# Kernel tuning notes

Measured on AMD Instinct MI355X. Metric: run time of the kernel, lower is better.

## Reference

```python
import jax, jax.numpy as jnp
import numpy as np

DT = 0.1          # sampling interval
DJ = 0.125        # scale resolution
W0 = 6.0          # Morlet omega0 (f0=6 -> deltaj0=0.6 in module)
DELTAJ0 = 0.6
WINDOW = 32
WS = WINDOW * 3 - 2  # sliding window size = 94

# rect window used in scale-smoothing (pycwt.rect): ones with half-weight ends, normalized
_wsize = int(round(DELTAJ0 / DJ * 2))  # 10
_win = np.ones(_wsize, np.float32)
_win[0] = _win[-1] = 0.5
_win /= _win.sum()


def _scales(n):
    # Morlet minimum scale s.t. Fourier period == 2*dt (wavelets_pytorch convention)
    s0 = 2.0 * DT * (W0 + np.sqrt(2.0 + W0 ** 2)) / (4.0 * np.pi)
    J = int((1.0 / DJ) * np.log2(n * DT / s0))
    return (s0 * 2.0 ** (DJ * np.arange(J + 1))).astype(np.float32)


def _cwt(y, scales, nfft):
    # Torrence & Compo FFT-based Morlet CWT. y: [n] real -> [S, n] complex
    n = y.shape[0]
    w = (2.0 * np.pi * np.fft.fftfreq(nfft, d=DT)).astype(np.float32)
    yh = jnp.fft.fft(y, n=nfft)                                  # [nfft]
    sw = scales[:, None] * w[None, :]                            # [S, nfft]
    psi_hat = (np.pi ** -0.25) * jnp.exp(-0.5 * (sw - W0) ** 2) * (w[None, :] > 0)
    norm = jnp.sqrt(2.0 * np.pi * scales[:, None] / DT)          # unit-energy normalization
    return jnp.fft.ifft(yh[None, :] * (norm * psi_hat), axis=1)[:, :n]


def _smooth(Wm, scales, nfft, real):
    # time smoothing: Gaussian filter in Fourier domain per scale (padded fft)
    n = Wm.shape[1]
    k2 = ((2.0 * np.pi * np.fft.fftfreq(nfft)).astype(np.float32)) ** 2
    F = jnp.exp(-0.5 * (scales[:, None] / DT) ** 2 * k2[None, :])  # [S, nfft]
    T = jnp.fft.ifft(F * jnp.fft.fft(Wm, n=nfft, axis=1), axis=1)[:, :n]
    if real:
        T = T.real
    # scale smoothing: boxcar-with-half-ends, 'same' convolution along scale axis
    win = jnp.asarray(_win).astype(T.dtype)
    return jax.vmap(lambda col: jnp.convolve(col, win, mode='same'),
                    in_axes=1, out_axes=1)(T)


def _wct(y1, y2, scales, nfft):
    y1 = (y1 - y1.mean()) / y1.std()
    y2 = (y2 - y2.mean()) / y2.std()
    W1 = _cwt(y1, scales, nfft)
    W2 = _cwt(y2, scales, nfft)
    inv_s = 1.0 / scales[:, None]
    S1 = _smooth(jnp.abs(W1) ** 2 * inv_s, scales, nfft, real=True)
    S2 = _smooth(jnp.abs(W2) ** 2 * inv_s, scales, nfft, real=True)
    S12 = _smooth(W1 * jnp.conj(W2) * inv_s, scales, nfft, real=False)
    wct = jnp.abs(S12) ** 2 / (S1 * S2)
    return wct.sum(axis=0)  # [n] coherence summed over scales


def setup_inputs() -> dict:
    key = jax.random.key(0)
    x = jax.random.normal(key, (64, 2, 2048), dtype=jnp.float32)
    return {"x": x}


def reference(x):
    n = x.shape[-1]
    nfft = int(2 ** np.ceil(np.log2(n)))  # pycwt fft_kwargs: next power of two
    scales = jnp.asarray(_scales(n))
    coh = jax.vmap(lambda p: _wct(p[0], p[1], scales, nfft))(x)   # [B, n]
    # sliding-window sum (unfold(0, WS, 1).sum(dim=1)) via cumsum
    cs = jnp.pad(jnp.cumsum(coh, axis=1), ((0, 0), (1, 0)))
    return cs[:, WS:] - cs[:, :-WS]                               # [B, n - WS + 1]
```

## Files before the change

kernel.cpp:

```cpp
#include <hip/hip_runtime.h>
#include <math.h>

#define N        2048
#define NT       256
#define NSC      81
#define BATCH    64
#define WS_WIN   94
#define NOUT     1955
#define DT_S     0.1f
#define W0_C     6.0f
#define PI_F     3.14159265358979f
#define TWOPI_F  6.28318530717959f
#define PIM14    0.7511255444649425f
#define C_SQ2H   0.70710678118654752f

#define SWZ(e)   ((e) + ((e) >> 4))
#define LDSN     2176

typedef float f4v __attribute__((ext_vector_type(4)));

__device__ __forceinline__ float4 ntload4(const float4* p) {
    f4v t = __builtin_nontemporal_load((const f4v*)p);
    return make_float4(t.x, t.y, t.z, t.w);
}
__device__ __forceinline__ void ntstore4(float4* p, float4 v) {
    f4v t; t.x = v.x; t.y = v.y; t.z = v.z; t.w = v.w;
    __builtin_nontemporal_store(t, (f4v*)p);
}

__device__ __forceinline__ float2 cadd2(float2 a, float2 b) { return make_float2(a.x + b.x, a.y + b.y); }
__device__ __forceinline__ float2 csub2(float2 a, float2 b) { return make_float2(a.x - b.x, a.y - b.y); }
__device__ __forceinline__ float2 cmul2(float2 a, float2 b) { return make_float2(a.x * b.x - a.y * b.y, a.x * b.y + a.y * b.x); }

struct Tw { float2 w[3][7]; };

__device__ __forceinline__ void tw_init(Tw& tw, int tid) {
    const int jm0 = tid, jm1 = tid & ~7, jm2 = tid & ~63;
    const int jms[3] = { jm0, jm1, jm2 };
    #pragma unroll
    for (int t = 0; t < 3; ++t) {
        float ang = -(TWOPI_F / (float)N) * (float)jms[t];
        float sn, cs; __sincosf(ang, &sn, &cs);
        float2 w1 = make_float2(cs, sn);
        tw.w[t][0] = w1;
        #pragma unroll
        for (int p = 1; p < 7; ++p) tw.w[t][p] = cmul2(tw.w[t][p - 1], w1);
    }
}

template<int SGN>
__device__ __forceinline__ float2 cmul_tw(float2 a, float2 w) {
    if (SGN < 0) return make_float2(a.x * w.x - a.y * w.y, a.x * w.y + a.y * w.x);
    else         return make_float2(a.x * w.x + a.y * w.y, a.y * w.x - a.x * w.y);
}

template<int SGN, bool HALF>
__device__ __forceinline__ void dft8(const float2 (&x)[8], float2 (&y)[8]) {
    const float s = (float)SGN;
    float2 t0, t1, t2, t3, u0, d1, d2, d3;
    if (HALF) {
        t0 = x[0]; t1 = x[1]; t2 = x[2]; t3 = x[3];
        u0 = x[0]; d1 = x[1]; d2 = x[2]; d3 = x[3];
    } else {
        t0 = cadd2(x[0], x[4]); t1 = cadd2(x[1], x[5]);
        t2 = cadd2(x[2], x[6]); t3 = cadd2(x[3], x[7]);
        u0 = csub2(x[0], x[4]);
        d1 = csub2(x[1], x[5]);
        d2 = csub2(x[2], x[6]);
        d3 = csub2(x[3], x[7]);
    }
    float2 u1 = make_float2(C_SQ2H * (d1.x - s * d1.y), C_SQ2H * (d1.y + s * d1.x));
    float2 u2 = make_float2(-s * d2.y, s * d2.x);
    float2 u3 = make_float2(-C_SQ2H * (d3.x + s * d3.y), C_SQ2H * (s * d3.x - d3.y));
    float2 a0 = cadd2(t0, t2), a1 = cadd2(t1, t3), b0 = csub2(t0, t2), e1 = csub2(t1, t3);
    float2 b1 = make_float2(-s * e1.y, s * e1.x);
    y[0] = cadd2(a0, a1); y[4] = csub2(a0, a1); y[2] = cadd2(b0, b1); y[6] = csub2(b0, b1);
    float2 c0 = cadd2(u0, u2), c1 = cadd2(u1, u3), g0 = csub2(u0, u2), h1 = csub2(u1, u3);
    float2 g1 = make_float2(-s * h1.y, s * h1.x);
    y[1] = cadd2(c0, c1); y[5] = csub2(c0, c1); y[3] = cadd2(g0, g1); y[7] = csub2(g0, g1);
}

template<int SGN>
__device__ __forceinline__ void twiddle_store(const float2 (&y)[8], float2* __restrict__ dst,
                                              const float2 (&w)[7], int base, int m) {
    dst[SWZ(base)] = y[0];
    #pragma unroll
    for (int p = 1; p < 8; ++p)
        dst[SWZ(base + p * m)] = cmul_tw<SGN>(y[p], w[p - 1]);
}

template<int SGN, bool HALF>
__device__ __forceinline__ void stage1_reg(const float2 (&x)[8], float2* __restrict__ dst,
                                           const Tw& tw, int tid) {
    float2 y[8];
    dft8<SGN, HALF>(x, y);
    twiddle_store<SGN>(y, dst, tw.w[0], 8 * tid, 1);
}

__device__ __forceinline__ void stage_read(const float2* __restrict__ src, float2 (&x)[8], int q) {
    #pragma unroll
    for (int p = 0; p < 8; ++p) x[p] = src[SWZ(q + p * 256)];
}

template<int SGN, int TWS>
__device__ __forceinline__ void stage_write(float2* __restrict__ dst, const float2 (&x)[8],
                                            const Tw& tw, int q) {
    float2 y[8];
    dft8<SGN, false>(x, y);
    const int m  = (TWS == 1) ? 8 : 64;
    const int jm = q & ~(m - 1);
    twiddle_store<SGN>(y, dst, tw.w[TWS], q + 7 * jm, m);
}

template<int SGN>
__device__ __forceinline__ void stage4_regs(const float2* __restrict__ src, float2 (&x)[8], int tid) {
    const float s = (float)SGN;
    #pragma unroll
    for (int qq = 0; qq < 2; ++qq) {
        int q = tid + qq * 256;
        float2 x0 = src[SWZ(q)];
        float2 x1 = src[SWZ(q + 512)];
        float2 x2 = src[SWZ(q + 1024)];
        float2 x3 = src[SWZ(q + 1536)];
        float2 a0 = cadd2(x0, x2), a1 = cadd2(x1, x3);
        float2 b0 = csub2(x0, x2), e1 = csub2(x1, x3);
        float2 b1 = make_float2(-s * e1.y, s * e1.x);
        x[0 + qq] = cadd2(a0, a1);
        x[2 + qq] = cadd2(b0, b1);
        x[4 + qq] = csub2(a0, a1);
        x[6 + qq] = csub2(b0, b1);
    }
}

template<int SGN, bool HALF>
__device__ __forceinline__ void fft2048_dual(float2 (&u)[8], float2 (&v)[8],
                                             float2* U, float2* V, const Tw& tw, int tid) {
    __syncthreads();
    stage1_reg<SGN, HALF>(u, U, tw, tid);
    stage1_reg<SGN, HALF>(v, V, tw, tid);
    __syncthreads();
    float2 xu[8], xv[8];
    stage_read(U, xu, tid);
    stage_read(V, xv, tid);
    __syncthreads();
    stage_write<SGN, 1>(U, xu, tw, tid);
    stage_write<SGN, 1>(V, xv, tw, tid);
    __syncthreads();
    stage_read(U, xu, tid);
    stage_read(V, xv, tid);
    __syncthreads();
    stage_write<SGN, 2>(U, xu, tw, tid);
    stage_write<SGN, 2>(V, xv, tw, tid);
    __syncthreads();
    stage4_regs<SGN>(U, u, tid);
    stage4_regs<SGN>(V, v, tid);
}

template<int SGN>
__device__ __forceinline__ void fft2048_single(float2 (&u)[8], float2* U, const Tw& tw, int tid) {
    __syncthreads();
    stage1_reg<SGN, false>(u, U, tw, tid);
    __syncthreads();
    float2 x[8];
    stage_read(U, x, tid);
    __syncthreads();
    stage_write<SGN, 1>(U, x, tw, tid);
    __syncthreads();
    stage_read(U, x, tid);
    __syncthreads();
    stage_write<SGN, 2>(U, x, tw, tid);
    __syncthreads();
    stage4_regs<SGN>(U, u, tid);
}

__global__ __launch_bounds__(NT) void k_fft_in(const float* __restrict__ x,
                                               float2* __restrict__ spec) {
    __shared__ float2 A[LDSN];
    __shared__ float  rs[NT], rq[NT];
    const int    tid = threadIdx.x;
    const float* y   = x + (size_t)blockIdx.x * N;

    Tw tw; tw_init(tw, tid);

    float v[8];
    float lsum = 0.f, lsq = 0.f;
    #pragma unroll
    for (int i = 0; i < 8; ++i) {
        float t = y[tid + i * NT];
        v[i] = t; lsum += t; lsq += t * t;
    }
    rs[tid] = lsum; rq[tid] = lsq;
    __syncthreads();
    for (int o = NT / 2; o > 0; o >>= 1) {
        if (tid < o) { rs[tid] += rs[tid + o]; rq[tid] += rq[tid + o]; }
        __syncthreads();
    }
    const float mean = rs[0] * (1.f / N);
    const float var  = rq[0] * (1.f / N) - mean * mean;
    const float inv  = rsqrtf(var);

    float2 z[8];
    #pragma unroll
    for (int i = 0; i < 8; ++i) z[i] = make_float2((v[i] - mean) * inv, 0.f);

    fft2048_single<-1>(z, A, tw, tid);

    float2* o2 = spec + (size_t)blockIdx.x * N;
    #pragma unroll
    for (int i = 0; i < 8; ++i) o2[tid + i * NT] = z[i];
}

__global__ __launch_bounds__(NT, 3) void k_wct(const float2* __restrict__ spec,
                                               float4* __restrict__ T, int b0) {
    __shared__ float2 U[LDSN];
    __shared__ float2 V[LDSN];
    const int tid  = threadIdx.x;
    const int sidx = blockIdx.x % NSC;
    const int bl   = blockIdx.x / NSC;
    const int b    = b0 + bl;

    Tw tw; tw_init(tw, tid);

    const float s0    = 2.f * DT_S * (W0_C + sqrtf(2.f + W0_C * W0_C)) / (4.f * PI_F);
    const float s     = s0 * exp2f(0.125f * (float)sidx);
    const float inv_s = 1.f / s;

    const float2* yh1 = spec + (size_t)(b * 2 + 0) * N;
    const float2* yh2 = spec + (size_t)(b * 2 + 1) * N;

    const float nrm   = PIM14 * sqrtf(TWOPI_F * s / DT_S) * (1.f / N);
    const float wstep = TWOPI_F / ((float)N * DT_S);

    float2 w1[8], w2[8];
    #pragma unroll
    for (int i = 0; i < 4; ++i) {
        int   k = tid + i * NT;
        float f = 0.f;
        if (k >= 1) {
            float arg = s * (wstep * (float)k) - W0_C;
            f = nrm * expf(-0.5f * arg * arg);
        }
        float2 a = yh1[k];
        float2 c = yh2[k];
        w1[i] = make_float2(a.x * f, a.y * f);
        w2[i] = make_float2(c.x * f, c.y * f);
    }
    #pragma unroll
    for (int i = 4; i < 8; ++i) {
        w1[i] = make_float2(0.f, 0.f);
        w2[i] = make_float2(0.f, 0.f);
    }
    fft2048_dual<+1, true>(w1, w2, U, V, tw, tid);

    float2 P[8], C[8];
    #pragma unroll
    for (int i = 0; i < 8; ++i) {
        float2 a = w1[i], c = w2[i];
        P[i] = make_float2((a.x * a.x + a.y * a.y) * inv_s,
                           (c.x * c.x + c.y * c.y) * inv_s);
        C[i] = make_float2((a.x * c.x + a.y * c.y) * inv_s,
                           (a.y * c.x - a.x * c.y) * inv_s);
    }

    const float sdt = s / DT_S;
    const float fc  = -0.5f * sdt * sdt * (TWOPI_F / (float)N) * (TWOPI_F / (float)N);

    fft2048_dual<-1, false>(P, C, U, V, tw, tid);

    #pragma unroll
    for (int i = 0; i < 8; ++i) {
        int   k  = tid + i * NT;
        int   mk = min(k, N - k);
        float F  = expf(fc * (float)(mk * mk)) * (1.f / N);
        P[i].x *= F; P[i].y *= F;
        C[i].x *= F; C[i].y *= F;
    }

    fft2048_dual<+1, false>(P, C, U, V, tw, tid);

    float4* To = T + ((size_t)bl * NSC + sidx) * N;
    #pragma unroll
    for (int i = 0; i < 8; ++i) {
        int k = tid + i * NT;
        ntstore4(&To[k], make_float4(P[i].x, P[i].y, C[i].x, C[i].y));
    }
}

__global__ __launch_bounds__(NT) void k_coh(const float4* __restrict__ T,
                                            float* __restrict__ coh, int b0) {
    const int bl = blockIdx.x >> 3;
    const int t  = ((blockIdx.x & 7) << 8) + threadIdx.x;
    const int b  = b0 + bl;
    const float4* col = T + (size_t)bl * NSC * N + t;

    float4 q[10];
    #pragma unroll
    for (int i = 0; i < 10; ++i) q[i] = make_float4(0.f, 0.f, 0.f, 0.f);
    #pragma unroll
    for (int i = 0; i < 5; ++i) q[5 + i] = ntload4(&col[(size_t)i * N]);

    float acc = 0.f;
    const float w9 = 1.f / 9.f;
    for (int i = 0; i < NSC; ++i) {
        float sx = 0.f, sy = 0.f, sz = 0.f, sw = 0.f;
        #pragma unroll
        for (int k = 0; k < 10; ++k) { sx += q[k].x; sy += q[k].y; sz += q[k].z; sw += q[k].w; }
        float s1 = (sx - 0.5f * (q[0].x + q[9].x)) * w9;
        float s2 = (sy - 0.5f * (q[0].y + q[9].y)) * w9;
        float sr = (sz - 0.5f * (q[0].z + q[9].z)) * w9;
        float si = (sw - 0.5f * (q[0].w + q[9].w)) * w9;
        acc += (sr * sr + si * si) / (s1 * s2);
        #pragma unroll
        for (int k = 0; k < 9; ++k) q[k] = q[k + 1];
        int c = i + 5;
        q[9] = (c < NSC) ? ntload4(&col[(size_t)c * N]) : make_float4(0.f, 0.f, 0.f, 0.f);
    }
    coh[(size_t)b * N + t] = acc;
}

__global__ __launch_bounds__(NT) void k_win(const float* __restrict__ coh,
                                            float* __restrict__ out) {
    __shared__ float row[N];
    const int b   = blockIdx.x;
    const int tid = threadIdx.x;
    for (int i = tid; i < N; i += NT) row[i] = coh[(size_t)b * N + i];
    __syncthreads();
    for (int t0 = tid; t0 < NOUT; t0 += NT) {
        float ssum = 0.f;
        for (int k = 0; k < WS_WIN; ++k) ssum += row[t0 + k];
        out[(size_t)b * NOUT + t0] = ssum;
    }
}

extern "C" void kernel_launch(void* const* d_in, const int* in_sizes, int n_in,
                              void* d_out, int out_size, void* d_ws, size_t ws_size,
                              hipStream_t stream) {
    const float* x   = (const float*)d_in[0];
    float*       out = (float*)d_out;
    char*        ws  = (char*)d_ws;

    const size_t spec_bytes = (size_t)BATCH * 2 * N * sizeof(float2);
    const size_t coh_bytes  = (size_t)BATCH * N * sizeof(float);
    const size_t perBatchT  = (size_t)NSC * N * sizeof(float4);

    float2* spec = (float2*)ws;
    float*  coh  = (float*)(ws + spec_bytes);
    float4* T    = (float4*)(ws + spec_bytes + coh_bytes);

    size_t avail = (ws_size > spec_bytes + coh_bytes) ? (ws_size - spec_bytes - coh_bytes) : 0;
    int chunk = (int)(avail / perBatchT);
    if (chunk < 1) chunk = 1;
    if (chunk > BATCH) chunk = BATCH;

    k_fft_in<<<BATCH * 2, NT, 0, stream>>>(x, spec);
    for (int b0 = 0; b0 < BATCH; b0 += chunk) {
        int cb = BATCH - b0 < chunk ? BATCH - b0 : chunk;
        k_wct<<<cb * NSC, NT, 0, stream>>>(spec, T, b0);
        k_coh<<<cb * 8, NT, 0, stream>>>(T, coh, b0);
    }
    k_win<<<BATCH, NT, 0, stream>>>(coh, out);
}
```

Baseline: 187.8 us.

## Vectorize complex math, split coherence scale loop, use prefix-sum sliding window

Complex arithmetic is rewritten with 2-wide float vectors so the compiler can emit packed FP32 ops in the FFTs. The k_coh scale loop is split into two halves per column, doubling the block count, with a deeper prefetch queue; the two partial sums go to separate buffers. k_win now builds a block-wide prefix sum and takes differences instead of summing 94 elements per output, and the input-normalization reduction uses wave shuffles. Together these target low occupancy in k_coh and redundant work in the small kernels, at the cost of extra workspace and a second coherence buffer.

```diff
diff --git a/kernel.cpp b/kernel.cpp
--- a/kernel.cpp
+++ b/kernel.cpp
@@ -18,6 +18,7 @@
 #define LDSN     2176
 
 typedef float f4v __attribute__((ext_vector_type(4)));
+typedef float f2 __attribute__((ext_vector_type(2)));
 
 __device__ __forceinline__ float4 ntload4(const float4* p) {
     f4v t = __builtin_nontemporal_load((const f4v*)p);
@@ -28,61 +29,68 @@
     __builtin_nontemporal_store(t, (f4v*)p);
 }
 
-__device__ __forceinline__ float2 cadd2(float2 a, float2 b) { return make_float2(a.x + b.x, a.y + b.y); }
-__device__ __forceinline__ float2 csub2(float2 a, float2 b) { return make_float2(a.x - b.x, a.y - b.y); }
-__device__ __forceinline__ float2 cmul2(float2 a, float2 b) { return make_float2(a.x * b.x - a.y * b.y, a.x * b.y + a.y * b.x); }
-
-struct Tw { float2 w[3][7]; };
+__device__ __forceinline__ f2 shxx(f2 a) { return __builtin_shufflevector(a, a, 0, 0); }
+__device__ __forceinline__ f2 shyy(f2 a) { return __builtin_shufflevector(a, a, 1, 1); }
+__device__ __forceinline__ f2 shyx(f2 a) { return __builtin_shufflevector(a, a, 1, 0); }
+
+template<int SGN>
+__device__ __forceinline__ f2 rot90(f2 d) {
+    return shyx(d) * (f2){ -(float)SGN, (float)SGN };
+}
+
+__device__ __forceinline__ f2 cmul(f2 a, f2 b) {
+    f2 t = shxx(a) * b;
+    f2 u = shyy(a) * shyx(b);
+    return t + u * (f2){ -1.f, 1.f };
+}
+
+template<int SGN>
+__device__ __forceinline__ f2 cmul_tw(f2 a, f2 w) {
+    f2 t = shxx(a) * w;
+    f2 u = shyy(a) * shyx(w);
+    if (SGN < 0) return t + u * (f2){ -1.f, 1.f };
+    else         return u + t * (f2){ 1.f, -1.f };
+}
+
+struct Tw { f2 w[3][7]; };
 
 __device__ __forceinline__ void tw_init(Tw& tw, int tid) {
-    const int jm0 = tid, jm1 = tid & ~7, jm2 = tid & ~63;
-    const int jms[3] = { jm0, jm1, jm2 };
+    const int jms[3] = { tid, tid & ~7, tid & ~63 };
     #pragma unroll
     for (int t = 0; t < 3; ++t) {
         float ang = -(TWOPI_F / (float)N) * (float)jms[t];
         float sn, cs; __sincosf(ang, &sn, &cs);
-        float2 w1 = make_float2(cs, sn);
+        f2 w1 = { cs, sn };
         tw.w[t][0] = w1;
         #pragma unroll
-        for (int p = 1; p < 7; ++p) tw.w[t][p] = cmul2(tw.w[t][p - 1], w1);
-    }
-}
-
-template<int SGN>
-__device__ __forceinline__ float2 cmul_tw(float2 a, float2 w) {
-    if (SGN < 0) return make_float2(a.x * w.x - a.y * w.y, a.x * w.y + a.y * w.x);
-    else         return make_float2(a.x * w.x + a.y * w.y, a.y * w.x - a.x * w.y);
+        for (int p = 1; p < 7; ++p) tw.w[t][p] = cmul(tw.w[t][p - 1], w1);
+    }
 }
 
 template<int SGN, bool HALF>
-__device__ __forceinline__ void dft8(const float2 (&x)[8], float2 (&y)[8]) {
-    const float s = (float)SGN;
-    float2 t0, t1, t2, t3, u0, d1, d2, d3;
+__device__ __forceinline__ void dft8(const f2 (&x)[8], f2 (&y)[8]) {
+    f2 t0, t1, t2, t3, u0, d1, d2, d3;
     if (HALF) {
         t0 = x[0]; t1 = x[1]; t2 = x[2]; t3 = x[3];
         u0 = x[0]; d1 = x[1]; d2 = x[2]; d3 = x[3];
     } else {
-        t0 = cadd2(x[0], x[4]); t1 = cadd2(x[1], x[5]);
-        t2 = cadd2(x[2], x[6]); t3 = cadd2(x[3], x[7]);
-        u0 = csub2(x[0], x[4]);
-        d1 = csub2(x[1], x[5]);
-        d2 = csub2(x[2], x[6]);
-        d3 = csub2(x[3], x[7]);
-    }
-    float2 u1 = make_float2(C_SQ2H * (d1.x - s * d1.y), C_SQ2H * (d1.y + s * d1.x));
-    float2 u2 = make_float2(-s * d2.y, s * d2.x);
-    float2 u3 = make_float2(-C_SQ2H * (d3.x + s * d3.y), C_SQ2H * (s * d3.x - d3.y));
-    float2 a0 = cadd2(t0, t2), a1 = cadd2(t1, t3), b0 = csub2(t0, t2), e1 = csub2(t1, t3);
-    float2 b1 = make_float2(-s * e1.y, s * e1.x);
-    y[0] = cadd2(a0, a1); y[4] = csub2(a0, a1); y[2] = cadd2(b0, b1); y[6] = csub2(b0, b1);
-    float2 c0 = cadd2(u0, u2), c1 = cadd2(u1, u3), g0 = csub2(u0, u2), h1 = csub2(u1, u3);
-    float2 g1 = make_float2(-s * h1.y, s * h1.x);
-    y[1] = cadd2(c0, c1); y[5] = csub2(c0, c1); y[3] = cadd2(g0, g1); y[7] = csub2(g0, g1);
+        t0 = x[0] + x[4]; t1 = x[1] + x[5]; t2 = x[2] + x[6]; t3 = x[3] + x[7];
+        u0 = x[0] - x[4]; d1 = x[1] - x[5]; d2 = x[2] - x[6]; d3 = x[3] - x[7];
+    }
+    f2 u1 = (d1 + rot90<SGN>(d1)) * C_SQ2H;
+    f2 u2 = rot90<SGN>(d2);
+    f2 u3 = (rot90<SGN>(d3) - d3) * C_SQ2H;
+    f2 a0 = t0 + t2, a1 = t1 + t3, b0 = t0 - t2, e1 = t1 - t3;
+    f2 b1 = rot90<SGN>(e1);
+    y[0] = a0 + a1; y[4] = a0 - a1; y[2] = b0 + b1; y[6] = b0 - b1;
+    f2 c0 = u0 + u2, c1 = u1 + u3, g0 = u0 - u2, h1 = u1 - u3;
+    f2 g1 = rot90<SGN>(h1);
+    y[1] = c0 + c1; y[5] = c0 - c1; y[3] = g0 + g1; y[7] = g0 - g1;
 }
 
 template<int SGN>
-__device__ __forceinline__ void twiddle_store(const float2 (&y)[8], float2* __restrict__ dst,
-                                              const float2 (&w)[7], int base, int m) {
+__device__ __forceinline__ void twiddle_store(const f2 (&y)[8], f2* __restrict__ dst,
+                                              const f2 (&w)[7], int base, int m) {
     dst[SWZ(base)] = y[0];
     #pragma unroll
     for (int p = 1; p < 8; ++p)
@@ -90,22 +98,22 @@
 }
 
 template<int SGN, bool HALF>
-__device__ __forceinline__ void stage1_reg(const float2 (&x)[8], float2* __restrict__ dst,
+__device__ __forceinline__ void stage1_reg(const f2 (&x)[8], f2* __restrict__ dst,
                                            const Tw& tw, int tid) {
-    float2 y[8];
+    f2 y[8];
     dft8<SGN, HALF>(x, y);
     twiddle_store<SGN>(y, dst, tw.w[0], 8 * tid, 1);
 }
 
-__device__ __forceinline__ void stage_read(const float2* __restrict__ src, float2 (&x)[8], int q) {
+__device__ __forceinline__ void stage_read(const f2* __restrict__ src, f2 (&x)[8], int q) {
     #pragma unroll
     for (int p = 0; p < 8; ++p) x[p] = src[SWZ(q + p * 256)];
 }
 
 template<int SGN, int TWS>
-__device__ __forceinline__ void stage_write(float2* __restrict__ dst, const float2 (&x)[8],
+__device__ __forceinline__ void stage_write(f2* __restrict__ dst, const f2 (&x)[8],
                                             const Tw& tw, int q) {
-    float2 y[8];
+    f2 y[8];
     dft8<SGN, false>(x, y);
     const int m  = (TWS == 1) ? 8 : 64;
     const int jm = q & ~(m - 1);
@@ -113,33 +121,31 @@
 }
 
 template<int SGN>
-__device__ __forceinline__ void stage4_regs(const float2* __restrict__ src, float2 (&x)[8], int tid) {
-    const float s = (float)SGN;
+__device__ __forceinline__ void stage4_regs(const f2* __restrict__ src, f2 (&x)[8], int tid) {
     #pragma unroll
     for (int qq = 0; qq < 2; ++qq) {
         int q = tid + qq * 256;
-        float2 x0 = src[SWZ(q)];
-        float2 x1 = src[SWZ(q + 512)];
-        float2 x2 = src[SWZ(q + 1024)];
-        float2 x3 = src[SWZ(q + 1536)];
-        float2 a0 = cadd2(x0, x2), a1 = cadd2(x1, x3);
-        float2 b0 = csub2(x0, x2), e1 = csub2(x1, x3);
-        float2 b1 = make_float2(-s * e1.y, s * e1.x);
-        x[0 + qq] = cadd2(a0, a1);
-        x[2 + qq] = cadd2(b0, b1);
-        x[4 + qq] = csub2(a0, a1);
-        x[6 + qq] = csub2(b0, b1);
+        f2 x0 = src[SWZ(q)];
+        f2 x1 = src[SWZ(q + 512)];
+        f2 x2 = src[SWZ(q + 1024)];
+        f2 x3 = src[SWZ(q + 1536)];
+        f2 a0 = x0 + x2, a1 = x1 + x3, b0 = x0 - x2, e1 = x1 - x3;
+        f2 b1 = rot90<SGN>(e1);
+        x[0 + qq] = a0 + a1;
+        x[2 + qq] = b0 + b1;
+        x[4 + qq] = a0 - a1;
+        x[6 + qq] = b0 - b1;
     }
 }
 
 template<int SGN, bool HALF>
-__device__ __forceinline__ void fft2048_dual(float2 (&u)[8], float2 (&v)[8],
-                                             float2* U, float2* V, const Tw& tw, int tid) {
+__device__ __forceinline__ void fft2048_dual(f2 (&u)[8], f2 (&v)[8],
+                                             f2* U, f2* V, const Tw& tw, int tid) {
     __syncthreads();
     stage1_reg<SGN, HALF>(u, U, tw, tid);
     stage1_reg<SGN, HALF>(v, V, tw, tid);
     __syncthreads();
-    float2 xu[8], xv[8];
+    f2 xu[8], xv[8];
     stage_read(U, xu, tid);
     stage_read(V, xv, tid);
     __syncthreads();
@@ -157,11 +163,11 @@
 }
 
 template<int SGN>
-__device__ __forceinline__ void fft2048_single(float2 (&u)[8], float2* U, const Tw& tw, int tid) {
+__device__ __forceinline__ void fft2048_single(f2 (&u)[8], f2* U, const Tw& tw, int tid) {
     __syncthreads();
     stage1_reg<SGN, false>(u, U, tw, tid);
     __syncthreads();
-    float2 x[8];
+    f2 x[8];
     stage_read(U, x, tid);
     __syncthreads();
     stage_write<SGN, 1>(U, x, tw, tid);
@@ -174,9 +180,9 @@
 }
 
 __global__ __launch_bounds__(NT) void k_fft_in(const float* __restrict__ x,
-                                               float2* __restrict__ spec) {
-    __shared__ float2 A[LDSN];
-    __shared__ float  rs[NT], rq[NT];
+                                               f2* __restrict__ spec) {
+    __shared__ f2 A[LDSN];
+    __shared__ float rs[4], rq[4];
     const int    tid = threadIdx.x;
     const float* y   = x + (size_t)blockIdx.x * N;
 
@@ -189,31 +195,35 @@
         float t = y[tid + i * NT];
         v[i] = t; lsum += t; lsq += t * t;
     }
-    rs[tid] = lsum; rq[tid] = lsq;
-    __syncthreads();
-    for (int o = NT / 2; o > 0; o >>= 1) {
-        if (tid < o) { rs[tid] += rs[tid + o]; rq[tid] += rq[tid + o]; }
-        __syncthreads();
-    }
-    const float mean = rs[0] * (1.f / N);
-    const float var  = rq[0] * (1.f / N) - mean * mean;
+    #pragma unroll
+    for (int o = 1; o < 64; o <<= 1) {
+        lsum += __shfl_xor(lsum, o, 64);
+        lsq  += __shfl_xor(lsq,  o, 64);
+    }
+    const int wid = tid >> 6, lane = tid & 63;
+    if (lane == 0) { rs[wid] = lsum; rq[wid] = lsq; }
+    __syncthreads();
+    const float fsum = rs[0] + rs[1] + rs[2] + rs[3];
+    const float fsq  = rq[0] + rq[1] + rq[2] + rq[3];
+    const float mean = fsum * (1.f / N);
+    const float var  = fsq * (1.f / N) - mean * mean;
     const float inv  = rsqrtf(var);
 
-    float2 z[8];
-    #pragma unroll
-    for (int i = 0; i < 8; ++i) z[i] = make_float2((v[i] - mean) * inv, 0.f);
+    f2 z[8];
+    #pragma unroll
+    for (int i = 0; i < 8; ++i) z[i] = (f2){ (v[i] - mean) * inv, 0.f };
 
     fft2048_single<-1>(z, A, tw, tid);
 
-    float2* o2 = spec + (size_t)blockIdx.x * N;
+    f2* o2 = spec + (size_t)blockIdx.x * N;
     #pragma unroll
     for (int i = 0; i < 8; ++i) o2[tid + i * NT] = z[i];
 }
 
-__global__ __launch_bounds__(NT, 3) void k_wct(const float2* __restrict__ spec,
+__global__ __launch_bounds__(NT, 3) void k_wct(const f2* __restrict__ spec,
                                                float4* __restrict__ T, int b0) {
-    __shared__ float2 U[LDSN];
-    __shared__ float2 V[LDSN];
+    __shared__ f2 U[LDSN];
+    __shared__ f2 V[LDSN];
     const int tid  = threadIdx.x;
     const int sidx = blockIdx.x % NSC;
     const int bl   = blockIdx.x / NSC;
@@ -225,13 +235,13 @@
     const float s     = s0 * exp2f(0.125f * (float)sidx);
     const float inv_s = 1.f / s;
 
-    const float2* yh1 = spec + (size_t)(b * 2 + 0) * N;
-    const float2* yh2 = spec + (size_t)(b * 2 + 1) * N;
+    const f2* yh1 = spec + (size_t)(b * 2 + 0) * N;
+    const f2* yh2 = spec + (size_t)(b * 2 + 1) * N;
 
     const float nrm   = PIM14 * sqrtf(TWOPI_F * s / DT_S) * (1.f / N);
     const float wstep = TWOPI_F / ((float)N * DT_S);
 
-    float2 w1[8], w2[8];
+    f2 w1[8], w2[8];
     #pragma unroll
     for (int i = 0; i < 4; ++i) {
         int   k = tid + i * NT;
@@ -240,26 +250,23 @@
             float arg = s * (wstep * (float)k) - W0_C;
             f = nrm * expf(-0.5f * arg * arg);
         }
-        float2 a = yh1[k];
-        float2 c = yh2[k];
-        w1[i] = make_float2(a.x * f, a.y * f);
-        w2[i] = make_float2(c.x * f, c.y * f);
+        w1[i] = yh1[k] * f;
+        w2[i] = yh2[k] * f;
     }
     #pragma unroll
     for (int i = 4; i < 8; ++i) {
-        w1[i] = make_float2(0.f, 0.f);
-        w2[i] = make_float2(0.f, 0.f);
+        w1[i] = (f2){ 0.f, 0.f };
+        w2[i] = (f2){ 0.f, 0.f };
     }
     fft2048_dual<+1, true>(w1, w2, U, V, tw, tid);
 
-    float2 P[8], C[8];
+    f2 P[8], C[8];
     #pragma unroll
     for (int i = 0; i < 8; ++i) {
-        float2 a = w1[i], c = w2[i];
-        P[i] = make_float2((a.x * a.x + a.y * a.y) * inv_s,
-                           (c.x * c.x + c.y * c.y) * inv_s);
-        C[i] = make_float2((a.x * c.x + a.y * c.y) * inv_s,
-                           (a.y * c.x - a.x * c.y) * inv_s);
+        f2 a = w1[i], c = w2[i];
+        f2 aa = a * a, cc = c * c;
+        P[i] = (f2){ aa.x + aa.y, cc.x + cc.y } * inv_s;
+        C[i] = cmul_tw<+1>(a, c) * inv_s;
     }
 
     const float sdt = s / DT_S;
@@ -272,8 +279,8 @@
         int   k  = tid + i * NT;
         int   mk = min(k, N - k);
         float F  = expf(fc * (float)(mk * mk)) * (1.f / N);
-        P[i].x *= F; P[i].y *= F;
-        C[i].x *= F; C[i].y *= F;
+        P[i] *= F;
+        C[i] *= F;
     }
 
     fft2048_dual<+1, false>(P, C, U, V, tw, tid);
@@ -288,20 +295,35 @@
 
 __global__ __launch_bounds__(NT) void k_coh(const float4* __restrict__ T,
                                             float* __restrict__ coh, int b0) {
-    const int bl = blockIdx.x >> 3;
-    const int t  = ((blockIdx.x & 7) << 8) + threadIdx.x;
-    const int b  = b0 + bl;
+    const int bl   = blockIdx.x >> 4;
+    const int r    = blockIdx.x & 15;
+    const int tile = r & 7;
+    const int g    = r >> 3;
+    const int t    = (tile << 8) + threadIdx.x;
+    const int b    = b0 + bl;
     const float4* col = T + (size_t)bl * NSC * N + t;
 
+    const int a    = g * 41;
+    const int bEnd = (g == 0) ? 41 : NSC;
+
     float4 q[10];
     #pragma unroll
-    for (int i = 0; i < 10; ++i) q[i] = make_float4(0.f, 0.f, 0.f, 0.f);
-    #pragma unroll
-    for (int i = 0; i < 5; ++i) q[5 + i] = ntload4(&col[(size_t)i * N]);
+    for (int k = 0; k < 10; ++k) {
+        int idx = a - 5 + k;
+        q[k] = (idx >= 0 && idx < NSC) ? ntload4(&col[(size_t)idx * N])
+                                       : make_float4(0.f, 0.f, 0.f, 0.f);
+    }
+    float4 p[4];
+    #pragma unroll
+    for (int j = 0; j < 4; ++j) {
+        int idx = a + 5 + j;
+        p[j] = (idx < NSC) ? ntload4(&col[(size_t)idx * N])
+                           : make_float4(0.f, 0.f, 0.f, 0.f);
+    }
 
     float acc = 0.f;
     const float w9 = 1.f / 9.f;
-    for (int i = 0; i < NSC; ++i) {
+    for (int i = a; i < bEnd; ++i) {
         float sx = 0.f, sy = 0.f, sz = 0.f, sw = 0.f;
         #pragma unroll
         for (int k = 0; k < 10; ++k) { sx += q[k].x; sy += q[k].y; sz += q[k].z; sw += q[k].w; }
@@ -312,24 +334,47 @@
         acc += (sr * sr + si * si) / (s1 * s2);
         #pragma unroll
         for (int k = 0; k < 9; ++k) q[k] = q[k + 1];
-        int c = i + 5;
-        q[9] = (c < NSC) ? ntload4(&col[(size_t)c * N]) : make_float4(0.f, 0.f, 0.f, 0.f);
-    }
-    coh[(size_t)b * N + t] = acc;
+        q[9] = p[0];
+        #pragma unroll
+        for (int j = 0; j < 3; ++j) p[j] = p[j + 1];
+        int c = i + 9;
+        p[3] = (c < NSC) ? ntload4(&col[(size_t)c * N]) : make_float4(0.f, 0.f, 0.f, 0.f);
+    }
+    coh[((size_t)g * BATCH + b) * N + t] = acc;
 }
 
 __global__ __launch_bounds__(NT) void k_win(const float* __restrict__ coh,
                                             float* __restrict__ out) {
-    __shared__ float row[N];
+    __shared__ float cs[N + 1];
+    __shared__ float tot[NT];
     const int b   = blockIdx.x;
     const int tid = threadIdx.x;
-    for (int i = tid; i < N; i += NT) row[i] = coh[(size_t)b * N + i];
-    __syncthreads();
-    for (int t0 = tid; t0 < NOUT; t0 += NT) {
-        float ssum = 0.f;
-        for (int k = 0; k < WS_WIN; ++k) ssum += row[t0 + k];
-        out[(size_t)b * NOUT + t0] = ssum;
-    }
+    const float* r0 = coh + (size_t)b * N;
+    const float* r1 = coh + (size_t)(BATCH + b) * N;
+
+    float v[8];
+    #pragma unroll
+    for (int j = 0; j < 8; ++j) {
+        int i = tid * 8 + j;
+        v[j] = r0[i] + r1[i];
+    }
+    #pragma unroll
+    for (int j = 1; j < 8; ++j) v[j] += v[j - 1];
+    tot[tid] = v[7];
+    __syncthreads();
+    for (int o = 1; o < NT; o <<= 1) {
+        float tv = (tid >= o) ? tot[tid - o] : 0.f;
+        __syncthreads();
+        tot[tid] += tv;
+        __syncthreads();
+    }
+    const float off = (tid > 0) ? tot[tid - 1] : 0.f;
+    if (tid == 0) cs[0] = 0.f;
+    #pragma unroll
+    for (int j = 0; j < 8; ++j) cs[tid * 8 + j + 1] = off + v[j];
+    __syncthreads();
+    for (int t0 = tid; t0 < NOUT; t0 += NT)
+        out[(size_t)b * NOUT + t0] = cs[t0 + WS_WIN] - cs[t0];
 }
 
 extern "C" void kernel_launch(void* const* d_in, const int* in_sizes, int n_in,
@@ -339,11 +384,11 @@
     float*       out = (float*)d_out;
     char*        ws  = (char*)d_ws;
 
-    const size_t spec_bytes = (size_t)BATCH * 2 * N * sizeof(float2);
-    const size_t coh_bytes  = (size_t)BATCH * N * sizeof(float);
+    const size_t spec_bytes = (size_t)BATCH * 2 * N * sizeof(f2);
+    const size_t coh_bytes  = (size_t)2 * BATCH * N * sizeof(float);
     const size_t perBatchT  = (size_t)NSC * N * sizeof(float4);
 
-    float2* spec = (float2*)ws;
+    f2*     spec = (f2*)ws;
     float*  coh  = (float*)(ws + spec_bytes);
     float4* T    = (float4*)(ws + spec_bytes + coh_bytes);
 
@@ -356,7 +401,7 @@
     for (int b0 = 0; b0 < BATCH; b0 += chunk) {
         int cb = BATCH - b0 < chunk ? BATCH - b0 : chunk;
         k_wct<<<cb * NSC, NT, 0, stream>>>(spec, T, b0);
-        k_coh<<<cb * 8, NT, 0, stream>>>(T, coh, b0);
+        k_coh<<<cb * 16, NT, 0, stream>>>(T, coh, b0);
     }
     k_win<<<BATCH, NT, 0, stream>>>(coh, out);
 }
```

After: 187.8 us. About the same (-0.0%).

## Split coherence scale loop, prefix-sum window, shuffle reductions, fast exp, higher occupancy

Applied to the files above, without the earlier changes.

The coherence kernel now splits the 81-scale loop into two halves per column, doubling the block count, and prefetches four rows ahead so global-load latency overlaps the arithmetic. The two partial sums are added in the window kernel, which now uses a block prefix sum instead of a 94-tap direct loop. The input normalisation uses wave shuffles instead of a shared-memory tree, the FFT kernel uses __expf, and its launch bound asks for 4 blocks per CU. The costs are doubled coh workspace, some rows reloaded where the halves overlap, possible register spills from the tighter launch bound, and small accuracy loss from fast exp and the cumsum difference.

```diff
diff --git a/kernel.cpp b/kernel.cpp
--- a/kernel.cpp
+++ b/kernel.cpp
@@ -35,8 +35,7 @@
 struct Tw { float2 w[3][7]; };
 
 __device__ __forceinline__ void tw_init(Tw& tw, int tid) {
-    const int jm0 = tid, jm1 = tid & ~7, jm2 = tid & ~63;
-    const int jms[3] = { jm0, jm1, jm2 };
+    const int jms[3] = { tid, tid & ~7, tid & ~63 };
     #pragma unroll
     for (int t = 0; t < 3; ++t) {
         float ang = -(TWOPI_F / (float)N) * (float)jms[t];
@@ -176,7 +175,7 @@
 __global__ __launch_bounds__(NT) void k_fft_in(const float* __restrict__ x,
                                                float2* __restrict__ spec) {
     __shared__ float2 A[LDSN];
-    __shared__ float  rs[NT], rq[NT];
+    __shared__ float rs[4], rq[4];
     const int    tid = threadIdx.x;
     const float* y   = x + (size_t)blockIdx.x * N;
 
@@ -189,14 +188,18 @@
         float t = y[tid + i * NT];
         v[i] = t; lsum += t; lsq += t * t;
     }
-    rs[tid] = lsum; rq[tid] = lsq;
-    __syncthreads();
-    for (int o = NT / 2; o > 0; o >>= 1) {
-        if (tid < o) { rs[tid] += rs[tid + o]; rq[tid] += rq[tid + o]; }
-        __syncthreads();
-    }
-    const float mean = rs[0] * (1.f / N);
-    const float var  = rq[0] * (1.f / N) - mean * mean;
+    #pragma unroll
+    for (int o = 1; o < 64; o <<= 1) {
+        lsum += __shfl_xor(lsum, o, 64);
+        lsq  += __shfl_xor(lsq,  o, 64);
+    }
+    const int wid = tid >> 6, lane = tid & 63;
+    if (lane == 0) { rs[wid] = lsum; rq[wid] = lsq; }
+    __syncthreads();
+    const float fsum = rs[0] + rs[1] + rs[2] + rs[3];
+    const float fsq  = rq[0] + rq[1] + rq[2] + rq[3];
+    const float mean = fsum * (1.f / N);
+    const float var  = fsq * (1.f / N) - mean * mean;
     const float inv  = rsqrtf(var);
 
     float2 z[8];
@@ -210,7 +213,7 @@
     for (int i = 0; i < 8; ++i) o2[tid + i * NT] = z[i];
 }
 
-__global__ __launch_bounds__(NT, 3) void k_wct(const float2* __restrict__ spec,
+__global__ __launch_bounds__(NT, 4) void k_wct(const float2* __restrict__ spec,
                                                float4* __restrict__ T, int b0) {
     __shared__ float2 U[LDSN];
     __shared__ float2 V[LDSN];
@@ -238,7 +241,7 @@
         float f = 0.f;
         if (k >= 1) {
             float arg = s * (wstep * (float)k) - W0_C;
-            f = nrm * expf(-0.5f * arg * arg);
+            f = nrm * __expf(-0.5f * arg * arg);
         }
         float2 a = yh1[k];
         float2 c = yh2[k];
@@ -271,7 +274,7 @@
     for (int i = 0; i < 8; ++i) {
         int   k  = tid + i * NT;
         int   mk = min(k, N - k);
-        float F  = expf(fc * (float)(mk * mk)) * (1.f / N);
+        float F  = __expf(fc * (float)(mk * mk)) * (1.f / N);
         P[i].x *= F; P[i].y *= F;
         C[i].x *= F; C[i].y *= F;
     }
@@ -288,20 +291,35 @@
 
 __global__ __launch_bounds__(NT) void k_coh(const float4* __restrict__ T,
                                             float* __restrict__ coh, int b0) {
-    const int bl = blockIdx.x >> 3;
-    const int t  = ((blockIdx.x & 7) << 8) + threadIdx.x;
-    const int b  = b0 + bl;
+    const int bl   = blockIdx.x >> 4;
+    const int r    = blockIdx.x & 15;
+    const int tile = r & 7;
+    const int g    = r >> 3;
+    const int t    = (tile << 8) + threadIdx.x;
+    const int b    = b0 + bl;
     const float4* col = T + (size_t)bl * NSC * N + t;
 
+    const int a    = g * 41;
+    const int bEnd = (g == 0) ? 41 : NSC;
+
     float4 q[10];
     #pragma unroll
-    for (int i = 0; i < 10; ++i) q[i] = make_float4(0.f, 0.f, 0.f, 0.f);
-    #pragma unroll
-    for (int i = 0; i < 5; ++i) q[5 + i] = ntload4(&col[(size_t)i * N]);
+    for (int k = 0; k < 10; ++k) {
+        int idx = a - 5 + k;
+        q[k] = (idx >= 0 && idx < NSC) ? ntload4(&col[(size_t)idx * N])
+                                       : make_float4(0.f, 0.f, 0.f, 0.f);
+    }
+    float4 p[4];
+    #pragma unroll
+    for (int j = 0; j < 4; ++j) {
+        int idx = a + 5 + j;
+        p[j] = (idx < NSC) ? ntload4(&col[(size_t)idx * N])
+                           : make_float4(0.f, 0.f, 0.f, 0.f);
+    }
 
     float acc = 0.f;
     const float w9 = 1.f / 9.f;
-    for (int i = 0; i < NSC; ++i) {
+    for (int i = a; i < bEnd; ++i) {
         float sx = 0.f, sy = 0.f, sz = 0.f, sw = 0.f;
         #pragma unroll
         for (int k = 0; k < 10; ++k) { sx += q[k].x; sy += q[k].y; sz += q[k].z; sw += q[k].w; }
@@ -312,24 +330,47 @@
         acc += (sr * sr + si * si) / (s1 * s2);
         #pragma unroll
         for (int k = 0; k < 9; ++k) q[k] = q[k + 1];
-        int c = i + 5;
-        q[9] = (c < NSC) ? ntload4(&col[(size_t)c * N]) : make_float4(0.f, 0.f, 0.f, 0.f);
-    }
-    coh[(size_t)b * N + t] = acc;
+        q[9] = p[0];
+        #pragma unroll
+        for (int j = 0; j < 3; ++j) p[j] = p[j + 1];
+        int c = i + 9;
+        p[3] = (c < NSC) ? ntload4(&col[(size_t)c * N]) : make_float4(0.f, 0.f, 0.f, 0.f);
+    }
+    coh[((size_t)g * BATCH + b) * N + t] = acc;
 }
 
 __global__ __launch_bounds__(NT) void k_win(const float* __restrict__ coh,
                                             float* __restrict__ out) {
-    __shared__ float row[N];
+    __shared__ float cs[N + 1];
+    __shared__ float tot[NT];
     const int b   = blockIdx.x;
     const int tid = threadIdx.x;
-    for (int i = tid; i < N; i += NT) row[i] = coh[(size_t)b * N + i];
-    __syncthreads();
-    for (int t0 = tid; t0 < NOUT; t0 += NT) {
-        float ssum = 0.f;
-        for (int k = 0; k < WS_WIN; ++k) ssum += row[t0 + k];
-        out[(size_t)b * NOUT + t0] = ssum;
-    }
+    const float* r0 = coh + (size_t)b * N;
+    const float* r1 = coh + (size_t)(BATCH + b) * N;
+
+    float v[8];
+    #pragma unroll
+    for (int j = 0; j < 8; ++j) {
+        int i = tid * 8 + j;
+        v[j] = r0[i] + r1[i];
+    }
+    #pragma unroll
+    for (int j = 1; j < 8; ++j) v[j] += v[j - 1];
+    tot[tid] = v[7];
+    __syncthreads();
+    for (int o = 1; o < NT; o <<= 1) {
+        float tv = (tid >= o) ? tot[tid - o] : 0.f;
+        __syncthreads();
+        tot[tid] += tv;
+        __syncthreads();
+    }
+    const float off = (tid > 0) ? tot[tid - 1] : 0.f;
+    if (tid == 0) cs[0] = 0.f;
+    #pragma unroll
+    for (int j = 0; j < 8; ++j) cs[tid * 8 + j + 1] = off + v[j];
+    __syncthreads();
+    for (int t0 = tid; t0 < NOUT; t0 += NT)
+        out[(size_t)b * NOUT + t0] = cs[t0 + WS_WIN] - cs[t0];
 }
 
 extern "C" void kernel_launch(void* const* d_in, const int* in_sizes, int n_in,
@@ -340,7 +381,7 @@
     char*        ws  = (char*)d_ws;
 
     const size_t spec_bytes = (size_t)BATCH * 2 * N * sizeof(float2);
-    const size_t coh_bytes  = (size_t)BATCH * N * sizeof(float);
+    const size_t coh_bytes  = (size_t)2 * BATCH * N * sizeof(float);
     const size_t perBatchT  = (size_t)NSC * N * sizeof(float4);
 
     float2* spec = (float2*)ws;
@@ -356,7 +397,7 @@
     for (int b0 = 0; b0 < BATCH; b0 += chunk) {
         int cb = BATCH - b0 < chunk ? BATCH - b0 : chunk;
         k_wct<<<cb * NSC, NT, 0, stream>>>(spec, T, b0);
-        k_coh<<<cb * 8, NT, 0, stream>>>(T, coh, b0);
+        k_coh<<<cb * 16, NT, 0, stream>>>(T, coh, b0);
     }
     k_win<<<BATCH, NT, 0, stream>>>(coh, out);
 }
```

Result: faster. 177.3 us (-5.6%).
